# Performance work log

Measured on AMD Instinct MI355X. Metric: run time of the kernel, lower is better.

## Reference

```python
import jax, jax.numpy as jnp
import numpy as np

# Mamba2 config (matches mamba_ssm.Mamba2 defaults used by the wrapper)
D_MODEL = 1024
D_STATE = 128
D_CONV = 4
EXPAND = 2
HEADDIM = 64
CHUNK = 256
D_INNER = EXPAND * D_MODEL            # 2048
NHEADS = D_INNER // HEADDIM           # 32
CONV_DIM = D_INNER + 2 * D_STATE      # 2304 (x, B, C share the causal conv)
D_IN_PROJ = 2 * D_INNER + 2 * D_STATE + NHEADS  # z, xBC, dt
EPS = 1e-5


def rmsnorm(x, w, eps=EPS):
    return x * jax.lax.rsqrt(jnp.mean(x * x, axis=-1, keepdims=True) + eps) * w


def setup_inputs() -> dict:
    key = jax.random.key(0)
    ks = jax.random.split(key, 8)
    B, L = 2, 2048
    def w(k, shape, sc=0.02):
        return jax.random.normal(k, shape, jnp.float32) * sc
    return {
        "x": jax.random.normal(ks[0], (B, L, D_MODEL), jnp.float32),
        "norm_w": jnp.ones((D_MODEL,), jnp.float32),
        "in_proj_w": w(ks[1], (D_IN_PROJ, D_MODEL)),
        "conv_w": w(ks[2], (CONV_DIM, 1, D_CONV), 0.2),   # depthwise kernel
        "conv_b": jnp.zeros((CONV_DIM,), jnp.float32),
        "dt_bias": w(ks[3], (NHEADS,), 1.0),
        "A_log": jnp.log(1.0 + 15.0 * jax.random.uniform(ks[4], (NHEADS,), jnp.float32)),
        "D": jnp.ones((NHEADS,), jnp.float32),
        "gnorm_w": jnp.ones((D_INNER,), jnp.float32),
        "out_proj_w": w(ks[5], (D_MODEL, D_INNER)),
    }


def _ssd(xd, a, Bm, Cm):
    """Chunked SSD scan (ssd_minimal_discrete).
    xd: (b,l,h,p) = x*dt ; a: (b,l,h) = dt*A ; Bm,Cm: (b,l,n) (ngroups=1)."""
    b, l, h, p = xd.shape
    n = Bm.shape[-1]
    nc = l // CHUNK
    xd = xd.reshape(b, nc, CHUNK, h, p)
    a = a.reshape(b, nc, CHUNK, h).transpose(0, 3, 1, 2)   # (b,h,nc,c)
    Bm = Bm.reshape(b, nc, CHUNK, n)
    Cm = Cm.reshape(b, nc, CHUNK, n)
    a_cs = jnp.cumsum(a, axis=-1)                           # (b,h,nc,c)
    # 1) intra-chunk: causal decay matrix L[t,s] = exp(sum_{s<i<=t} a_i)
    diff = a_cs[..., :, None] - a_cs[..., None, :]          # (b,h,nc,c,c)
    mask = jnp.tril(jnp.ones((CHUNK, CHUNK), bool))
    Lm = jnp.exp(jnp.where(mask, diff, 0.0)) * mask
    Y_diag = jnp.einsum("bcln,bcsn,bhcls,bcshp->bclhp", Cm, Bm, Lm, xd)
    # 2) per-chunk end states
    decay_states = jnp.exp(a_cs[..., -1:] - a_cs)           # (b,h,nc,c)
    states = jnp.einsum("bcln,bhcl,bclhp->bchpn", Bm, decay_states, xd)
    # 3) inter-chunk recurrence (vectorized segsum over the 8+1 chunk totals)
    tot = jnp.pad(a_cs[..., -1], ((0, 0), (0, 0), (1, 0)))  # (b,h,nc+1)
    tot_cs = jnp.cumsum(tot, axis=-1)
    dchunk = tot_cs[..., :, None] - tot_cs[..., None, :]    # (b,h,nc+1,nc+1)
    cmask = jnp.tril(jnp.ones((nc + 1, nc + 1), bool))
    dchunk = jnp.exp(jnp.where(cmask, dchunk, 0.0)) * cmask
    states = jnp.concatenate([jnp.zeros_like(states[:, :1]), states], axis=1)
    new_states = jnp.einsum("bhzc,bchpn->bzhpn", dchunk, states)
    init_states = new_states[:, :-1]                        # state entering each chunk
    # 4) state -> output contribution
    Y_off = jnp.einsum("bcln,bchpn,bhcl->bclhp", Cm, init_states, jnp.exp(a_cs))
    return (Y_diag + Y_off).reshape(b, l, h, p)


def reference(x, norm_w, in_proj_w, conv_w, conv_b, dt_bias, A_log, D, gnorm_w, out_proj_w):
    res = x
    u = rmsnorm(x, norm_w)
    zxbcdt = u @ in_proj_w.T                                # (b,l,d_in_proj)
    z, xBC, dt = jnp.split(zxbcdt, [D_INNER, D_INNER + CONV_DIM], axis=-1)
    # causal depthwise conv1d over (x,B,C), then SiLU
    xBC_t = jnp.pad(xBC.transpose(0, 2, 1), ((0, 0), (0, 0), (D_CONV - 1, 0)))
    conv = jax.lax.conv_general_dilated(
        xBC_t, conv_w, (1,), "VALID",
        dimension_numbers=("NCH", "OIH", "NCH"), feature_group_count=CONV_DIM)
    xBC = jax.nn.silu(conv.transpose(0, 2, 1) + conv_b)
    xs, Bm, Cm = jnp.split(xBC, [D_INNER, D_INNER + D_STATE], axis=-1)
    dt = jax.nn.softplus(dt + dt_bias)                      # (b,l,h)
    A = -jnp.exp(A_log)                                     # (h,)
    xh = xs.reshape(xs.shape[0], xs.shape[1], NHEADS, HEADDIM)
    y = _ssd(xh * dt[..., None], dt * A, Bm, Cm)
    y = y + D[None, None, :, None] * xh                     # skip term
    y = y.reshape(xs.shape)
    y = rmsnorm(y * jax.nn.silu(z), gnorm_w)                # gated RMSNorm
    return res + y @ out_proj_w.T
```

## Files before the change

kernel.cpp:

```cpp
#include <hip/hip_runtime.h>
#include <hip/hip_bf16.h>

typedef __hip_bfloat16 bf16_t;
typedef __attribute__((ext_vector_type(8))) short bfrag8;
typedef __attribute__((ext_vector_type(4))) float floatx4;

#define DM     1024
#define DI     2048
#define NHD    32
#define HD     64
#define DSTATE 128
#define CONVD  2304
#define NPROJ  4384
#define NPAD   4480
#define MR     4096
#define LL     2048
#define EPSF   1e-5f
#define LOG2E  1.44269504088896f

__device__ __forceinline__ void gl_lds16(const void* g, void* l) {
  __builtin_amdgcn_global_load_lds((const __attribute__((address_space(1))) void*)g,
                                   (__attribute__((address_space(3))) void*)l, 16, 0, 0);
}
__device__ __forceinline__ unsigned pack_bf16_rn(float a, float b) {
  unsigned ua = (__float_as_uint(a) + 0x8000u) >> 16;
  unsigned ub = (__float_as_uint(b) + 0x8000u) >> 16;
  return ua | (ub << 16);
}
__device__ __forceinline__ unsigned short bf16u(float a) {
  return (unsigned short)((__float_as_uint(a) + 0x8000u) >> 16);
}
__device__ __forceinline__ float blo(unsigned u){ return __uint_as_float(u << 16); }
__device__ __forceinline__ float bhi(unsigned u){ return __uint_as_float(u & 0xffff0000u); }
__device__ __forceinline__ void unp8(uint4 u, float* v) {
  v[0]=blo(u.x); v[1]=bhi(u.x); v[2]=blo(u.y); v[3]=bhi(u.y);
  v[4]=blo(u.z); v[5]=bhi(u.z); v[6]=blo(u.w); v[7]=bhi(u.w);
}
typedef union { unsigned u[4]; bfrag8 f; } fragu;

__global__ void rms1_kernel(const float* __restrict__ x, const float* __restrict__ w,
                            bf16_t* __restrict__ ub) {
  int row = blockIdx.x, t = threadIdx.x;
  float4 v = ((const float4*)(x + (long)row * DM))[t];
  float ss = v.x*v.x + v.y*v.y + v.z*v.z + v.w*v.w;
#pragma unroll
  for (int off = 32; off > 0; off >>= 1) ss += __shfl_down(ss, off, 64);
  __shared__ float red[4];
  if ((t & 63) == 0) red[t >> 6] = ss;
  __syncthreads();
  float tot = red[0] + red[1] + red[2] + red[3];
  float rs = rsqrtf(tot * (1.f / DM) + EPSF);
  float4 wv = ((const float4*)w)[t];
  bf16_t* o = ub + (long)row * DM + t * 4;
  o[0] = __float2bfloat16(v.x * rs * wv.x);
  o[1] = __float2bfloat16(v.y * rs * wv.y);
  o[2] = __float2bfloat16(v.z * rs * wv.z);
  o[3] = __float2bfloat16(v.w * rs * wv.w);
}

#define W1CNT (NPAD * DM / 4)
#define W2CNT (DM * DI / 4)
__global__ void cvtw_kernel(const float* __restrict__ w1, const float* __restrict__ w2,
                            const float* __restrict__ gw,
                            bf16_t* __restrict__ o1, bf16_t* __restrict__ o2) {
  int i4 = blockIdx.x * 256 + threadIdx.x;
  if (i4 < W1CNT) {
    int idx = i4 * 4;
    int row = idx >> 10;
    float4 v = make_float4(0.f, 0.f, 0.f, 0.f);
    if (row < NPROJ) v = *(const float4*)(w1 + idx);
    bf16_t* d = o1 + idx;
    d[0] = __float2bfloat16(v.x); d[1] = __float2bfloat16(v.y);
    d[2] = __float2bfloat16(v.z); d[3] = __float2bfloat16(v.w);
  } else {
    int idx = (i4 - W1CNT) * 4;
    int k = idx & (DI - 1);
    float4 v = *(const float4*)(w2 + idx);
    float4 g = *(const float4*)(gw + k);
    bf16_t* d = o2 + idx;
    d[0] = __float2bfloat16(v.x * g.x); d[1] = __float2bfloat16(v.y * g.y);
    d[2] = __float2bfloat16(v.z * g.z); d[3] = __float2bfloat16(v.w * g.w);
  }
}

template<int TN, bool DO_RES, bool OUT_BF16>
__global__ __launch_bounds__(256) void gemm64_kernel(const bf16_t* __restrict__ A,
    const bf16_t* __restrict__ Bw, const float* __restrict__ resid,
    const float* __restrict__ rs_row, void* __restrict__ Cout, int N, int K) {
  __shared__ bf16_t As[128 * 64];
  __shared__ bf16_t Bs[TN * 64];
  const int tid = threadIdx.x;
  const int lane = tid & 63;
  const int wv = tid >> 6;
  const int l15 = lane & 15;
  const int l4 = lane >> 4;
  constexpr int MF = (TN == 128) ? 4 : 2;
  const int wm = (TN == 128) ? ((wv >> 1) << 6) : (wv << 5);
  const int wn = (TN == 128) ? ((wv & 1) << 6) : 0;
  const int tm = blockIdx.x << 7;
  const int tn = blockIdx.y * TN;

  floatx4 acc[MF][4];
#pragma unroll
  for (int i = 0; i < MF; i++)
#pragma unroll
    for (int j = 0; j < 4; j++) acc[i][j] = (floatx4){0.f, 0.f, 0.f, 0.f};

  const int r = tid >> 3;
  const int c8 = tid & 7;
  const int scol = ((c8 ^ (r & 7)) << 3);
  const bf16_t* Ag = A + (long)(tm + r) * K + scol;
  const bf16_t* Bg = Bw + (long)(tn + r) * K + scol;
  const int swz = l15 & 7;

  for (int k0 = 0; k0 < K; k0 += 64) {
#pragma unroll
    for (int q = 0; q < 4; q++)
      gl_lds16(Ag + (long)(q * 32) * K + k0, &As[q * 2048 + tid * 8]);
#pragma unroll
    for (int q = 0; q < TN / 32; q++)
      gl_lds16(Bg + (long)(q * 32) * K + k0, &Bs[q * 2048 + tid * 8]);
    __syncthreads();
#pragma unroll
    for (int kk = 0; kk < 2; kk++) {
      bfrag8 af[MF], bfr[4];
      const int ch = ((kk << 2) | l4) ^ swz;
#pragma unroll
      for (int j = 0; j < 4; j++)
        bfr[j] = *(const bfrag8*)&Bs[(wn + j * 16 + l15) * 64 + ch * 8];
#pragma unroll
      for (int i = 0; i < MF; i++)
        af[i] = *(const bfrag8*)&As[(wm + i * 16 + l15) * 64 + ch * 8];
#pragma unroll
      for (int i = 0; i < MF; i++)
#pragma unroll
        for (int j = 0; j < 4; j++)
          acc[i][j] = __builtin_amdgcn_mfma_f32_16x16x32_bf16(af[i], bfr[j], acc[i][j], 0, 0, 0);
    }
    __syncthreads();
  }
#pragma unroll
  for (int i = 0; i < MF; i++)
#pragma unroll
    for (int j = 0; j < 4; j++)
#pragma unroll
      for (int r2 = 0; r2 < 4; r2++) {
        int row = tm + wm + i * 16 + l4 * 4 + r2;
        int col = tn + wn + j * 16 + l15;
        float v = acc[i][j][r2];
        if (OUT_BF16) {
          ((bf16_t*)Cout)[(long)row * N + col] = __float2bfloat16(v);
        } else {
          if (DO_RES) v = v * rs_row[row] + resid[(long)row * N + col];
          ((float*)Cout)[(long)row * N + col] = v;
        }
      }
}

__global__ __launch_bounds__(256) void gemm_s_kernel(const bf16_t* __restrict__ Cmh,
                const bf16_t* __restrict__ Bmh, float* __restrict__ SL) {
  __shared__ bf16_t As[128 * 32];
  __shared__ bf16_t Bs[128 * 32];
  const int tid = threadIdx.x;
  const int lane = tid & 63;
  const int wv = tid >> 6;
  const int wm = (wv >> 1) << 6;
  const int wn = (wv & 1) << 6;
  const int bc = blockIdx.z;
  const int tm = blockIdx.x << 7;
  const int tn = blockIdx.y << 7;
  const int l15 = lane & 15;
  const int l4 = lane >> 4;
  floatx4 acc[4][4];
#pragma unroll
  for (int i = 0; i < 4; i++)
#pragma unroll
    for (int j = 0; j < 4; j++) acc[i][j] = (floatx4){0.f, 0.f, 0.f, 0.f};
  const int arow = tid >> 2;
  const int acol = (tid & 3) << 3;
  const bf16_t* Ag = Cmh + (long)bc * 256 * DSTATE + (long)(tm + arow) * DSTATE + acol;
  const bf16_t* Bg = Bmh + (long)bc * 256 * DSTATE + (long)(tn + arow) * DSTATE + acol;
  const long k64 = (long)64 * DSTATE;
  for (int k0 = 0; k0 < DSTATE; k0 += 32) {
    gl_lds16(Ag + k0, &As[tid * 8]);
    gl_lds16(Ag + k64 + k0, &As[2048 + tid * 8]);
    gl_lds16(Bg + k0, &Bs[tid * 8]);
    gl_lds16(Bg + k64 + k0, &Bs[2048 + tid * 8]);
    __syncthreads();
    bfrag8 af[4], bfr[4];
#pragma unroll
    for (int i = 0; i < 4; i++)
      af[i] = *(const bfrag8*)&As[(wm + i * 16 + l15) * 32 + l4 * 8];
#pragma unroll
    for (int j = 0; j < 4; j++)
      bfr[j] = *(const bfrag8*)&Bs[(wn + j * 16 + l15) * 32 + l4 * 8];
#pragma unroll
    for (int i = 0; i < 4; i++)
#pragma unroll
      for (int j = 0; j < 4; j++)
        acc[i][j] = __builtin_amdgcn_mfma_f32_16x16x32_bf16(af[i], bfr[j], acc[i][j], 0, 0, 0);
    __syncthreads();
  }
  float* Cb = SL + (long)bc * 65536;
#pragma unroll
  for (int i = 0; i < 4; i++)
#pragma unroll
    for (int j = 0; j < 4; j++)
#pragma unroll
      for (int r = 0; r < 4; r++)
        Cb[(long)(tm + wm + i * 16 + l4 * 4 + r) * 256 + tn + wn + j * 16 + l15] = acc[i][j][r];
}

__global__ __launch_bounds__(256) void conv4_kernel(const bf16_t* __restrict__ zxh,
    const float* __restrict__ cw, const float* __restrict__ cb,
    bf16_t* __restrict__ xhb, bf16_t* __restrict__ Bmh, bf16_t* __restrict__ Cmh) {
  int g = blockIdx.x * 256 + threadIdx.x;
  int cg = g % 288;
  int blt = g / 288;
  int c0 = cg * 8;
  long bl0 = (long)blt * 4;
  int l0 = (int)(bl0 & (LL - 1));
  const bf16_t* base = zxh + bl0 * NPAD + DI + c0;
  float rv[7][8];
#pragma unroll
  for (int j = 0; j < 7; j++) {
    int dj = j - 3;
    if (l0 + dj >= 0) {
      uint4 u = *(const uint4*)(base + (long)dj * NPAD);
      unp8(u, rv[j]);
    } else {
#pragma unroll
      for (int q = 0; q < 8; q++) rv[j][q] = 0.f;
    }
  }
  float4 wq[8];
#pragma unroll
  for (int q = 0; q < 8; q++) wq[q] = ((const float4*)cw)[c0 + q];
  float bias[8];
  *(float4*)&bias[0] = *(const float4*)(cb + c0);
  *(float4*)&bias[4] = *(const float4*)(cb + c0 + 4);
#pragma unroll
  for (int i = 0; i < 4; i++) {
    unsigned o[4];
#pragma unroll
    for (int q2 = 0; q2 < 4; q2++) {
      float rr[2];
#pragma unroll
      for (int e = 0; e < 2; e++) {
        int q = q2 * 2 + e;
        float a = bias[q] + wq[q].x * rv[i][q] + wq[q].y * rv[i + 1][q]
                + wq[q].z * rv[i + 2][q] + wq[q].w * rv[i + 3][q];
        rr[e] = a / (1.f + __expf(-a));
      }
      o[q2] = pack_bf16_rn(rr[0], rr[1]);
    }
    uint4 ov = make_uint4(o[0], o[1], o[2], o[3]);
    long bl = bl0 + i;
    if (c0 < DI)               *(uint4*)(xhb + bl * DI + c0) = ov;
    else if (c0 < DI + DSTATE) *(uint4*)(Bmh + bl * DSTATE + (c0 - DI)) = ov;
    else                       *(uint4*)(Cmh + bl * DSTATE + (c0 - DI - DSTATE)) = ov;
  }
}

__global__ __launch_bounds__(256) void xdt_kernel(const bf16_t* __restrict__ xhb,
    const bf16_t* __restrict__ Bmh, const bf16_t* __restrict__ zxh,
    const float* __restrict__ A_log, const float* __restrict__ dtb,
    float* __restrict__ acs, float* __restrict__ ctot,
    bf16_t* __restrict__ xdT, bf16_t* __restrict__ xdTe, bf16_t* __restrict__ BmT) {
  __shared__ unsigned short Tb[9216];
  __shared__ float acsL[256];
  __shared__ float dtsL[256];
  __shared__ float wsum[4];
  int blk = blockIdx.x;
  int t = threadIdx.x;
  if (blk < 512) {
    int h = blk & 31, bc = blk >> 5;
    {
      int lane = t & 63, w = t >> 6;
      float Ah = -__expf(A_log[h]) * LOG2E;
      int gl = bc * 256 + t;
      float vv = __bfloat162float(zxh[(long)gl * NPAD + (NPROJ - 32) + h]) + dtb[h];
      float sp = fmaxf(vv, 0.f) + log1pf(__expf(-fabsf(vv)));
      float a = sp * Ah;
#pragma unroll
      for (int off = 1; off < 64; off <<= 1) {
        float v = __shfl_up(a, off, 64);
        if (lane >= off) a += v;
      }
      if (lane == 63) wsum[w] = a;
      __syncthreads();
      float base = 0.f;
      for (int i = 0; i < 4; i++) base += (i < w) ? wsum[i] : 0.f;
      a += base;
      acsL[t] = a;
      dtsL[t] = sp;
      acs[blk * 256 + t] = a;
      if (t == 255) ctot[blk] = a;
      __syncthreads();
    }
    float atot = acsL[255];
    unsigned short* T1 = Tb;
    unsigned short* T2 = Tb + 4608;
    int l_loc = t >> 2, pg = t & 3;
    for (int lt = 0; lt < 4; lt++) {
      int ll = lt * 64 + l_loc;
      int gl = bc * 256 + ll;
      float w1 = dtsL[ll];
      float w2 = w1 * exp2f(atot - acsL[ll]);
      const uint4* src = (const uint4*)(xhb + (long)gl * DI + h * HD + pg * 16);
      uint4 u0 = src[0], u1 = src[1];
      float v[16];
      unp8(u0, v); unp8(u1, v + 8);
      __syncthreads();
#pragma unroll
      for (int q = 0; q < 16; q++) {
        T1[(pg * 16 + q) * 72 + l_loc] = bf16u(v[q] * w1);
        T2[(pg * 16 + q) * 72 + l_loc] = bf16u(v[q] * w2);
      }
      __syncthreads();
      long orow = ((long)blk * 64 + l_loc) * 256 + lt * 64 + pg * 16;
      *(uint4*)(xdT + orow)      = *(uint4*)&T1[l_loc * 72 + pg * 16];
      *(uint4*)(xdT + orow + 8)  = *(uint4*)&T1[l_loc * 72 + pg * 16 + 8];
      *(uint4*)(xdTe + orow)     = *(uint4*)&T2[l_loc * 72 + pg * 16];
      *(uint4*)(xdTe + orow + 8) = *(uint4*)&T2[l_loc * 72 + pg * 16 + 8];
    }
  } else {
    unsigned short* T = Tb;
    int bc = blk - 512;
    int l_loc = t >> 2, ng = t & 3;
    for (int lt = 0; lt < 4; lt++) {
      int gl = bc * 256 + lt * 64 + l_loc;
      const uint4* src = (const uint4*)(Bmh + (long)gl * DSTATE + ng * 32);
      uint4 u[4];
#pragma unroll
      for (int q = 0; q < 4; q++) u[q] = src[q];
      __syncthreads();
      const unsigned short* us = (const unsigned short*)u;
#pragma unroll
      for (int e = 0; e < 32; e++)
        T[(ng * 32 + e) * 72 + l_loc] = us[e];
      __syncthreads();
      int n = t >> 1, lg2 = t & 1;
      long orow = ((long)bc * 128 + n) * 256 + lt * 64 + lg2 * 32;
#pragma unroll
      for (int q = 0; q < 4; q++)
        *(uint4*)(BmT + orow + q * 8) = *(uint4*)&T[n * 72 + lg2 * 32 + q * 8];
    }
  }
}

__global__ __launch_bounds__(256) void states3_kernel(const bf16_t* __restrict__ xdTe,
    const bf16_t* __restrict__ BmT, bf16_t* __restrict__ states) {
  int blk = blockIdx.x;
  int bc = blk >> 5;
  int t = threadIdx.x, lane = t & 63, wv = t >> 6;
  int l15 = lane & 15, l4 = lane >> 4;
  floatx4 acc[2][4];
#pragma unroll
  for (int i = 0; i < 2; i++)
#pragma unroll
    for (int j = 0; j < 4; j++) acc[i][j] = (floatx4){0.f, 0.f, 0.f, 0.f};
  const bf16_t* arow = BmT + (long)bc * 128 * 256;
  const bf16_t* brow = xdTe + (long)blk * 64 * 256;
#pragma unroll
  for (int kt = 0; kt < 8; kt++) {
    bfrag8 af[2], bfr[4];
#pragma unroll
    for (int i = 0; i < 2; i++)
      af[i] = *(const bfrag8*)(arow + (long)(wv * 32 + i * 16 + l15) * 256 + kt * 32 + l4 * 8);
#pragma unroll
    for (int j = 0; j < 4; j++)
      bfr[j] = *(const bfrag8*)(brow + (long)(j * 16 + l15) * 256 + kt * 32 + l4 * 8);
#pragma unroll
    for (int i = 0; i < 2; i++)
#pragma unroll
      for (int j = 0; j < 4; j++)
        acc[i][j] = __builtin_amdgcn_mfma_f32_16x16x32_bf16(af[i], bfr[j], acc[i][j], 0, 0, 0);
  }
#pragma unroll
  for (int i = 0; i < 2; i++)
#pragma unroll
    for (int j = 0; j < 4; j++) {
      int n_base = wv * 32 + i * 16 + l4 * 4;
      int p = j * 16 + l15;
      unsigned lo = pack_bf16_rn(acc[i][j][0], acc[i][j][1]);
      unsigned hi = pack_bf16_rn(acc[i][j][2], acc[i][j][3]);
      *(uint2*)(states + (long)blk * 8192 + p * 128 + n_base) = make_uint2(lo, hi);
    }
}

__global__ void scan_kernel(const bf16_t* __restrict__ states, const float* __restrict__ ctot,
                            bf16_t* __restrict__ initsb) {
  int id = blockIdx.x * 256 + threadIdx.x;
  int pn = id & 8191;
  int bh = id >> 13;
  int b = bh >> 5, h = bh & 31;
  float S = 0.f;
#pragma unroll
  for (int c = 0; c < 8; c++) {
    int blk = (b * 8 + c) * 32 + h;
    initsb[(long)blk * 8192 + pn] = __float2bfloat16(S);
    S = exp2f(ctot[blk]) * S + __bfloat162float(states[(long)blk * 8192 + pn]);
  }
}

__global__ __launch_bounds__(512, 4) void yk4_kernel(const float* __restrict__ SL,
     const bf16_t* __restrict__ Cmh, const bf16_t* __restrict__ xhb,
     const bf16_t* __restrict__ zxh, const float* __restrict__ acs,
     const bf16_t* __restrict__ initsb, const bf16_t* __restrict__ xdT,
     const float* __restrict__ Dp, bf16_t* __restrict__ yg, float* __restrict__ ssqp) {
  int bi = blockIdx.x;
  int bc = (bi & 7) * 2 + ((bi >> 3) & 1);
  int h = bi >> 4;
  int ablk = bc * 32 + h;
  int t = threadIdx.x;
  int wv = t >> 6;
  int mh = wv >> 2, wsub = wv & 3;
  int lane = t & 63;
  int l15 = lane & 15, l4 = lane >> 4;

  __shared__ float acsS[256];
  __shared__ __align__(16) char bbuf[49152];
  bf16_t* xds = (bf16_t*)bbuf;
  bf16_t* ins = (bf16_t*)(bbuf + 32768);
  float* Yt = (float*)bbuf;

  {
    const bf16_t* xrow_g = xdT + (long)ablk * 64 * 256;
#pragma unroll
    for (int it = 0; it < 4; it++) {
      int sl = it * 512 + t;
      int p = sl >> 5, s = sl & 31;
      int c = (s & 24) | ((s & 7) ^ (p & 7));
      gl_lds16(xrow_g + p * 256 + c * 8, &xds[sl * 8]);
    }
    const bf16_t* irow_g = initsb + (long)ablk * 8192;
#pragma unroll
    for (int it = 0; it < 2; it++) {
      int sl = it * 512 + t;
      int p = sl >> 4, s = sl & 15;
      int c = (s & 8) | ((s & 7) ^ (p & 7));
      gl_lds16(irow_g + p * 128 + c * 8, &ins[sl * 8]);
    }
  }
  if (t < 256) acsS[t] = acs[ablk * 256 + t];
  __syncthreads();

  const int rowbase = bc * 256;
  const int l0 = mh * 128 + wsub * 32 + l15;
  const int l1 = l0 + 16;
  const float al0 = acsS[l0], al1 = acsS[l1];
  const float eA0 = exp2f(al0), eA1 = exp2f(al1);
  const float* SL0 = SL + (long)bc * 65536 + (long)l0 * 256;
  const float* SL1 = SL + (long)bc * 65536 + (long)l1 * 256;

  floatx4 acc[2][4];
#pragma unroll
  for (int i = 0; i < 2; i++)
#pragma unroll
    for (int j = 0; j < 4; j++) acc[i][j] = (floatx4){0.f, 0.f, 0.f, 0.f};

  const int nkd = (mh + 1) * 4;
  for (int kt = 0; kt < nkd; kt++) {
    int sbase = kt * 32 + l4 * 8;
    float as[8];
    *(float4*)&as[0] = *(const float4*)&acsS[sbase];
    *(float4*)&as[4] = *(const float4*)&acsS[sbase + 4];
    float sv0[8], sv1[8];
    *(float4*)&sv0[0] = *(const float4*)(SL0 + sbase);
    *(float4*)&sv0[4] = *(const float4*)(SL0 + sbase + 4);
    *(float4*)&sv1[0] = *(const float4*)(SL1 + sbase);
    *(float4*)&sv1[4] = *(const float4*)(SL1 + sbase + 4);
    fragu af0, af1;
#pragma unroll
    for (int q2 = 0; q2 < 4; q2++) {
      float p00, p01, p10, p11;
      {
        int s = sbase + q2 * 2;
        float d0 = al0 - as[q2 * 2], d1 = al0 - as[q2 * 2 + 1];
        p00 = (s <= l0) ? sv0[q2 * 2] * exp2f(fminf(d0, 0.f)) : 0.f;
        p01 = (s + 1 <= l0) ? sv0[q2 * 2 + 1] * exp2f(fminf(d1, 0.f)) : 0.f;
        float e0 = al1 - as[q2 * 2], e1 = al1 - as[q2 * 2 + 1];
        p10 = (s <= l1) ? sv1[q2 * 2] * exp2f(fminf(e0, 0.f)) : 0.f;
        p11 = (s + 1 <= l1) ? sv1[q2 * 2 + 1] * exp2f(fminf(e1, 0.f)) : 0.f;
      }
      af0.u[q2] = pack_bf16_rn(p00, p01);
      af1.u[q2] = pack_bf16_rn(p10, p11);
    }
    bfrag8 bfr[4];
    int ch = kt * 4 + l4;
#pragma unroll
    for (int j = 0; j < 4; j++) {
      int p = j * 16 + l15;
      int sw = (ch & 24) | ((ch & 7) ^ (p & 7));
      bfr[j] = *(const bfrag8*)&xds[(p * 32 + sw) * 8];
    }
#pragma unroll
    for (int j = 0; j < 4; j++) {
      acc[0][j] = __builtin_amdgcn_mfma_f32_16x16x32_bf16(af0.f, bfr[j], acc[0][j], 0, 0, 0);
      acc[1][j] = __builtin_amdgcn_mfma_f32_16x16x32_bf16(af1.f, bfr[j], acc[1][j], 0, 0, 0);
    }
  }
#pragma unroll
  for (int kt = 0; kt < 4; kt++) {
    int n0 = kt * 32 + l4 * 8;
    uint4 c0 = *(const uint4*)(Cmh + (long)(rowbase + l0) * DSTATE + n0);
    uint4 c1 = *(const uint4*)(Cmh + (long)(rowbase + l1) * DSTATE + n0);
    float cv0[8], cv1[8];
    unp8(c0, cv0); unp8(c1, cv1);
    fragu af0, af1;
#pragma unroll
    for (int q2 = 0; q2 < 4; q2++) {
      af0.u[q2] = pack_bf16_rn(cv0[q2 * 2] * eA0, cv0[q2 * 2 + 1] * eA0);
      af1.u[q2] = pack_bf16_rn(cv1[q2 * 2] * eA1, cv1[q2 * 2 + 1] * eA1);
    }
    bfrag8 bfr[4];
    int ch = kt * 4 + l4;
#pragma unroll
    for (int j = 0; j < 4; j++) {
      int p = j * 16 + l15;
      int sw = (ch & 8) | ((ch & 7) ^ (p & 7));
      bfr[j] = *(const bfrag8*)&ins[(p * 16 + sw) * 8];
    }
#pragma unroll
    for (int j = 0; j < 4; j++) {
      acc[0][j] = __builtin_amdgcn_mfma_f32_16x16x32_bf16(af0.f, bfr[j], acc[0][j], 0, 0, 0);
      acc[1][j] = __builtin_amdgcn_mfma_f32_16x16x32_bf16(af1.f, bfr[j], acc[1][j], 0, 0, 0);
    }
  }
  float Dh = Dp[h];
#pragma unroll
  for (int pass = 0; pass < 2; pass++) {
    __syncthreads();
    if (mh == pass) {
#pragma unroll
      for (int i = 0; i < 2; i++)
#pragma unroll
        for (int j = 0; j < 4; j++)
#pragma unroll
          for (int r = 0; r < 4; r++)
            Yt[(wsub * 32 + i * 16 + l4 * 4 + r) * 66 + j * 16 + l15] = acc[i][j][r];
    }
    __syncthreads();
    {
      int row_l = t >> 2;
      int chc = (t & 3) * 16;
      long rowg = rowbase + pass * 128 + row_l;
      float ss = 0.f;
#pragma unroll
      for (int it = 0; it < 2; it++) {
        int c = chc + it * 8;
        float4 y0 = *(const float4*)&Yt[row_l * 66 + c];
        float4 y1 = *(const float4*)&Yt[row_l * 66 + c + 4];
        uint4 ux = *(const uint4*)(xhb + rowg * DI + h * HD + c);
        uint4 uz = *(const uint4*)(zxh + rowg * NPAD + h * HD + c);
        float xv[8], zv[8];
        unp8(ux, xv); unp8(uz, zv);
        float yv[8] = {y0.x, y0.y, y0.z, y0.w, y1.x, y1.y, y1.z, y1.w};
        unsigned o[4];
#pragma unroll
        for (int q = 0; q < 4; q++) {
          float v0 = (yv[q * 2 + 0] + Dh * xv[q * 2 + 0]) *
                     (zv[q * 2 + 0] / (1.f + __expf(-zv[q * 2 + 0])));
          float v1 = (yv[q * 2 + 1] + Dh * xv[q * 2 + 1]) *
                     (zv[q * 2 + 1] / (1.f + __expf(-zv[q * 2 + 1])));
          ss += v0 * v0 + v1 * v1;
          o[q] = pack_bf16_rn(v0, v1);
        }
        *(uint4*)(yg + rowg * DI + h * HD + c) = make_uint4(o[0], o[1], o[2], o[3]);
      }
      ss += __shfl_xor(ss, 1, 64);
      ss += __shfl_xor(ss, 2, 64);
      if ((t & 3) == 0) ssqp[rowg * 32 + h] = ss;
    }
  }
}

__global__ void rsred_kernel(const float* __restrict__ ssqp, float* __restrict__ rs) {
  int row = blockIdx.x * 256 + threadIdx.x;
  const float4* p = (const float4*)(ssqp + row * 32);
  float s = 0.f;
#pragma unroll
  for (int q = 0; q < 8; q++) {
    float4 v = p[q];
    s += v.x + v.y + v.z + v.w;
  }
  rs[row] = rsqrtf(s * (1.f / DI) + EPSF);
}

extern "C" void kernel_launch(void* const* d_in, const int* in_sizes, int n_in,
                              void* d_out, int out_size, void* d_ws, size_t ws_size,
                              hipStream_t stream) {
  const float* x    = (const float*)d_in[0];
  const float* nw   = (const float*)d_in[1];
  const float* w1   = (const float*)d_in[2];
  const float* cw   = (const float*)d_in[3];
  const float* cb   = (const float*)d_in[4];
  const float* dtb  = (const float*)d_in[5];
  const float* alog = (const float*)d_in[6];
  const float* Dp   = (const float*)d_in[7];
  const float* gw   = (const float*)d_in[8];
  const float* w2   = (const float*)d_in[9];
  float* out = (float*)d_out;

  char* ws = (char*)d_ws;
  size_t off = 0;
  auto alloc = [&](size_t bytes) -> void* {
    void* p = ws + off;
    off += (bytes + 255) & ~(size_t)255;
    return p;
  };
  bf16_t* ub     = (bf16_t*)alloc((size_t)MR * DM * 2);
  bf16_t* w1b    = (bf16_t*)alloc((size_t)NPAD * DM * 2);
  bf16_t* w2b    = (bf16_t*)alloc((size_t)DM * DI * 2);
  bf16_t* zxh    = (bf16_t*)alloc((size_t)MR * NPAD * 2);
  bf16_t* xhb    = (bf16_t*)alloc((size_t)MR * DI * 2);
  bf16_t* Bmh    = (bf16_t*)alloc((size_t)MR * DSTATE * 2);
  bf16_t* Cmh    = (bf16_t*)alloc((size_t)MR * DSTATE * 2);
  float* SL      = (float*)alloc((size_t)16 * 256 * 256 * 4);
  float* acs     = (float*)alloc((size_t)512 * 256 * 4);
  float* ctot    = (float*)alloc((size_t)512 * 4);
  bf16_t* states = (bf16_t*)alloc((size_t)512 * 8192 * 2);
  bf16_t* initsb = (bf16_t*)alloc((size_t)512 * 8192 * 2);
  bf16_t* xdT    = (bf16_t*)alloc((size_t)512 * 64 * 256 * 2);
  bf16_t* xdTe   = (bf16_t*)alloc((size_t)512 * 64 * 256 * 2);
  bf16_t* BmT    = (bf16_t*)alloc((size_t)16 * 128 * 256 * 2);
  bf16_t* yg     = (bf16_t*)alloc((size_t)MR * DI * 2);
  float* ssqp    = (float*)alloc((size_t)MR * NHD * 4);
  float* rs      = (float*)alloc((size_t)MR * 4);
  if (off > ws_size) return;

  rms1_kernel<<<MR, 256, 0, stream>>>(x, nw, ub);
  cvtw_kernel<<<(W1CNT + W2CNT) / 256, 256, 0, stream>>>(w1, w2, gw, w1b, w2b);
  gemm64_kernel<128, false, true><<<dim3(MR / 128, NPAD / 128), 256, 0, stream>>>(
      ub, w1b, nullptr, nullptr, zxh, NPAD, DM);
  conv4_kernel<<<(1024 * 288) / 256, 256, 0, stream>>>(zxh, cw, cb, xhb, Bmh, Cmh);
  xdt_kernel<<<528, 256, 0, stream>>>(xhb, Bmh, zxh, alog, dtb, acs, ctot, xdT, xdTe, BmT);
  gemm_s_kernel<<<dim3(2, 2, 16), 256, 0, stream>>>(Cmh, Bmh, SL);
  states3_kernel<<<512, 256, 0, stream>>>(xdTe, BmT, states);
  scan_kernel<<<(2 * 32 * 8192) / 256, 256, 0, stream>>>(states, ctot, initsb);
  yk4_kernel<<<512, 512, 0, stream>>>(SL, Cmh, xhb, zxh, acs, initsb, xdT, Dp, yg, ssqp);
  rsred_kernel<<<MR / 256, 256, 0, stream>>>(ssqp, rs);
  gemm64_kernel<64, true, false><<<dim3(MR / 128, DM / 64), 256, 0, stream>>>(
      yg, w2b, x, rs, out, DM, DI);
}
```

Before: 265.0 us.

## Add 256x256-tile pipelined GEMM for in_proj with remainder handled by old kernel

Replaces the in_proj GEMM's 128x128 tiling with a new 512-thread kernel that computes 256x256 output tiles. It stages A and B into 128KB of swizzled LDS via global_load_lds, double-buffers the loads, and interleaves them with MFMA phases using explicit waitcnt, barriers and setprio. Block indices are swizzled for L2 locality. The 4096 columns covered by full tiles go to the new kernel, and the remaining padded columns run through the old gemm64 kernel at 64-wide tiles. This aims to raise arithmetic intensity and overlap loads with compute, at the cost of a second launch and heavy LDS and register use.

```diff
diff --git a/kernel.cpp b/kernel.cpp
--- a/kernel.cpp
+++ b/kernel.cpp
@@ -154,6 +154,122 @@
           if (DO_RES) v = v * rs_row[row] + resid[(long)row * N + col];
           ((float*)Cout)[(long)row * N + col] = v;
         }
+      }
+}
+
+__global__ __launch_bounds__(512, 2) void gemm256_kernel(const bf16_t* __restrict__ A,
+    const bf16_t* __restrict__ Bw, bf16_t* __restrict__ Cout) {
+  __shared__ bf16_t lds[65536];
+  const int t = threadIdx.x;
+  const int lane = t & 63, wv = t >> 6;
+  const int wm = wv >> 2, wn = wv & 3;
+  const int l15 = lane & 15, l4 = lane >> 4;
+  const int flat = blockIdx.x;
+  const int swzb = (flat & 7) * 32 + (flat >> 3);
+  const int bx = swzb & 15, by = swzb >> 4;
+  const int tm = bx << 8, tn = by << 8;
+
+  const int srow = t >> 3;
+  const int scol = ((t & 7) ^ (srow & 7)) << 3;
+  const bf16_t* Ag = A + (long)(tm + srow) * DM + scol;
+  const bf16_t* Bg = Bw + (long)(tn + srow) * DM + scol;
+  bf16_t* Asl = lds;
+  bf16_t* Bsl = lds + 32768;
+  const int swl = (l15 & 7) << 4;
+  const int ca0 = (l4 * 16) ^ swl;
+  const int ca1 = (64 + l4 * 16) ^ swl;
+
+  floatx4 acc[8][4];
+#pragma unroll
+  for (int i = 0; i < 8; i++)
+#pragma unroll
+    for (int j = 0; j < 4; j++) acc[i][j] = (floatx4){0.f, 0.f, 0.f, 0.f};
+  bfrag8 bq[8];
+
+#define STG_A(tt, h) { \
+  bf16_t* d_ = Asl + (((tt) & 1) * 2 + (h)) * 8192 + t * 8; \
+  gl_lds16(Ag + (long)((h) * 128     ) * DM + (tt) * 64, d_); \
+  gl_lds16(Ag + (long)((h) * 128 + 64) * DM + (tt) * 64, d_ + 4096); \
+}
+#define STG_B(tt, h) { \
+  bf16_t* d_ = Bsl + (((tt) & 1) * 2 + (h)) * 8192 + t * 8; \
+  gl_lds16(Bg + (long)((h) * 128     ) * DM + (tt) * 64, d_); \
+  gl_lds16(Bg + (long)((h) * 128 + 64) * DM + (tt) * 64, d_ + 4096); \
+}
+#define PH(d, q, STG, WT) { \
+  const char* Ah_ = (const char*)(Asl + ((d) * 2 + wm) * 8192); \
+  const char* Bh_ = (const char*)(Bsl + ((d) * 2 + (wn >> 1)) * 8192); \
+  if ((q) == 0) { \
+    _Pragma("unroll") \
+    for (int j = 0; j < 4; j++) { \
+      int r_ = ((wn & 1) << 6) + j * 16 + l15; \
+      bq[j * 2]     = *(const bfrag8*)(Bh_ + r_ * 128 + ca0); \
+      bq[j * 2 + 1] = *(const bfrag8*)(Bh_ + r_ * 128 + ca1); \
+    } \
+  } \
+  bfrag8 aq0, aq1, aq2, aq3; \
+  { int r_ = (q) * 32 + l15; \
+    aq0 = *(const bfrag8*)(Ah_ + r_ * 128 + ca0); \
+    aq1 = *(const bfrag8*)(Ah_ + r_ * 128 + ca1); \
+    aq2 = *(const bfrag8*)(Ah_ + (r_ + 16) * 128 + ca0); \
+    aq3 = *(const bfrag8*)(Ah_ + (r_ + 16) * 128 + ca1); } \
+  STG; \
+  __builtin_amdgcn_s_barrier(); \
+  asm volatile("s_waitcnt lgkmcnt(0)" ::: "memory"); \
+  __builtin_amdgcn_s_setprio(1); \
+  _Pragma("unroll") \
+  for (int j = 0; j < 4; j++) { \
+    acc[(q)*2  ][j] = __builtin_amdgcn_mfma_f32_16x16x32_bf16(aq0, bq[j*2],   acc[(q)*2  ][j], 0, 0, 0); \
+    acc[(q)*2  ][j] = __builtin_amdgcn_mfma_f32_16x16x32_bf16(aq1, bq[j*2+1], acc[(q)*2  ][j], 0, 0, 0); \
+    acc[(q)*2+1][j] = __builtin_amdgcn_mfma_f32_16x16x32_bf16(aq2, bq[j*2],   acc[(q)*2+1][j], 0, 0, 0); \
+    acc[(q)*2+1][j] = __builtin_amdgcn_mfma_f32_16x16x32_bf16(aq3, bq[j*2+1], acc[(q)*2+1][j], 0, 0, 0); \
+  } \
+  __builtin_amdgcn_s_setprio(0); \
+  WT; \
+  __builtin_amdgcn_s_barrier(); \
+}
+
+  STG_A(0, 0); STG_A(0, 1); STG_B(0, 0); STG_B(0, 1);
+  STG_B(1, 0); STG_B(1, 1);
+  asm volatile("s_waitcnt vmcnt(4)" ::: "memory");
+  __builtin_amdgcn_s_barrier();
+
+  for (int it = 0; it < 7; ++it) {
+    const int ta = 2 * it, tb = ta + 1;
+    PH(0, 0, STG_A(tb, 0), {})
+    PH(0, 1, STG_A(tb, 1), {})
+    PH(0, 2, STG_B(ta + 2, 0), {})
+    PH(0, 3, STG_B(ta + 2, 1), asm volatile("s_waitcnt vmcnt(4)" ::: "memory");)
+    PH(1, 0, STG_A(ta + 2, 0), {})
+    PH(1, 1, STG_A(ta + 2, 1), {})
+    PH(1, 2, STG_B(tb + 2, 0), {})
+    PH(1, 3, STG_B(tb + 2, 1), asm volatile("s_waitcnt vmcnt(4)" ::: "memory");)
+  }
+  {
+    PH(0, 0, STG_A(15, 0), {})
+    PH(0, 1, STG_A(15, 1), {})
+    PH(0, 2, {}, {})
+    PH(0, 3, {}, asm volatile("s_waitcnt vmcnt(0)" ::: "memory");)
+    PH(1, 0, {}, {})
+    PH(1, 1, {}, {})
+    PH(1, 2, {}, {})
+    PH(1, 3, {}, {})
+  }
+#undef PH
+#undef STG_A
+#undef STG_B
+
+  const long crow = tm + wm * 128;
+  const int ccol = tn + wn * 64;
+#pragma unroll
+  for (int qi = 0; qi < 8; qi++)
+#pragma unroll
+    for (int j = 0; j < 4; j++)
+#pragma unroll
+      for (int r2 = 0; r2 < 4; r2++) {
+        long row = crow + (qi >> 1) * 32 + (qi & 1) * 16 + l4 * 4 + r2;
+        int col = ccol + j * 16 + l15;
+        Cout[row * NPAD + col] = __float2bfloat16(acc[qi][j][r2]);
       }
 }
 
@@ -632,8 +748,9 @@
 
   rms1_kernel<<<MR, 256, 0, stream>>>(x, nw, ub);
   cvtw_kernel<<<(W1CNT + W2CNT) / 256, 256, 0, stream>>>(w1, w2, gw, w1b, w2b);
-  gemm64_kernel<128, false, true><<<dim3(MR / 128, NPAD / 128), 256, 0, stream>>>(
-      ub, w1b, nullptr, nullptr, zxh, NPAD, DM);
+  gemm256_kernel<<<256, 512, 0, stream>>>(ub, w1b, zxh);
+  gemm64_kernel<64, false, true><<<dim3(MR / 128, 6), 256, 0, stream>>>(
+      ub, w1b + (size_t)4096 * DM, nullptr, nullptr, zxh + 4096, NPAD, DM);
   conv4_kernel<<<(1024 * 288) / 256, 256, 0, stream>>>(zxh, cw, cb, xhb, Bmh, Cmh);
   xdt_kernel<<<528, 256, 0, stream>>>(xhb, Bmh, zxh, alog, dtb, acs, ctot, xdT, xdTe, BmT);
   gemm_s_kernel<<<dim3(2, 2, 16), 256, 0, stream>>>(Cmh, Bmh, SL);
```

New measurement: 263.7 us. About the same (-0.5%).
